# Kernel optimization log

Measured on AMD Instinct MI355X. Metric: run time of the kernel, lower is better.

## Reference

```python
import jax, jax.numpy as jnp
import numpy as np

B, Q, R, D = 32, 512, 1024, 2048
L = Q + R
GAMMA, LMBDA, KL_COEFF = 0.99, 0.95, 0.1
PENALISE_NO_EOS = True
REWARD_PENALTY = -3.0
MIN_RESPONSE_LEN = 0
MAX_RESPONSE_LEN = 1024


def setup_inputs() -> dict:
    key = jax.random.key(0)
    k = jax.random.split(key, 6)
    hidden = jax.random.normal(k[0], (B, L, D), jnp.float32)
    w_base = jax.random.normal(k[1], (D,), jnp.float32) / np.float32(np.sqrt(D))
    w_adapter = jax.random.normal(k[2], (D,), jnp.float32) / np.float32(np.sqrt(D))
    gen_logprobs = jax.random.normal(k[3], (B, R), jnp.float32)
    ref_logprobs = jax.random.normal(k[4], (B, R), jnp.float32)
    # left-aligned responses: resp_lens real tokens then padding (True = pad).
    resp_lens = jax.random.randint(k[5], (B,), 1, R + 1)
    responses_pad_mask = jnp.arange(R)[None, :] >= resp_lens[:, None]
    return {"hidden": hidden, "w_base": w_base, "w_adapter": w_adapter,
            "gen_logprobs": gen_logprobs, "ref_logprobs": ref_logprobs,
            "responses_pad_mask": responses_pad_mask, "queries_len": Q}


def _gae(values, rewards):
    # backward-in-time GAE recurrence via lax.scan (reverse=True), vectorized over batch
    v_next = jnp.concatenate([values[:, 1:], jnp.zeros_like(values[:, :1])], axis=1)
    def step(carry, xs):
        v_t, r_t, vn_t = xs
        adv = r_t + GAMMA * vn_t - v_t + GAMMA * LMBDA * carry
        return adv, adv
    init = jnp.zeros(values.shape[0], values.dtype)
    _, advs = jax.lax.scan(step, init, (values.T, rewards.T, v_next.T), reverse=True)
    return advs.T  # [B, R]


def _masked_whiten(x, mask):
    # torchtune masked_whiten: masked mean/var (Bessel-corrected) over all masked entries
    m = mask.astype(x.dtype)
    n = jnp.sum(m)
    mean = jnp.sum(x * m) / n
    var = jnp.sum(((x - mean) ** 2) * m) / n
    var = var * (n / (n - 1.0))  # unbiased
    return (x - mean) * jax.lax.rsqrt(var + 1e-8)


def _forward(hidden, w_base, w_adapter, gen_logprobs, ref_logprobs,
             responses_pad_mask, queries_len):
    b = hidden.shape[0]
    # scorer with adapter -> values; scorer with adapter disabled -> scores
    values_full = jnp.einsum('bld,d->bl', hidden, w_base + w_adapter)
    scores_full = jnp.einsum('bld,d->bl', hidden, w_base)
    values = values_full[:, queries_len - 1:-1]  # [B, R]

    # index of last unmasked (non-pad) response token; 0 if fully padded
    response_last_pos = jnp.argmax(jnp.cumsum(~responses_pad_mask, axis=-1), axis=-1)

    scores = jnp.take_along_axis(
        scores_full, (response_last_pos + queries_len)[:, None], axis=1)[:, 0]

    penalty_mask = jnp.zeros((b,), bool)
    if PENALISE_NO_EOS:
        penalty_mask = penalty_mask | ~jnp.any(responses_pad_mask, axis=-1)
    if MIN_RESPONSE_LEN:
        penalty_mask = penalty_mask | (response_last_pos < MIN_RESPONSE_LEN)
    scores = jnp.where(penalty_mask, jnp.asarray(REWARD_PENALTY, scores.dtype), scores)

    value_last_pos = jnp.where(
        (response_last_pos > 0) & (response_last_pos < MAX_RESPONSE_LEN - 1),
        response_last_pos + 1, response_last_pos)
    value_pad_mask = responses_pad_mask.at[jnp.arange(b), value_last_pos].set(False)
    values = jnp.where(value_pad_mask, jnp.asarray(0.0, values.dtype), values)

    # get_rewards_ppo
    kl = gen_logprobs - ref_logprobs
    kl_rewards = -KL_COEFF * kl
    rewards = kl_rewards.at[jnp.arange(b), value_last_pos].add(scores)

    # estimate_advantages
    advantages = _gae(values, rewards)
    returns = advantages + values
    mask = ~responses_pad_mask
    advantages = jnp.where(mask, _masked_whiten(advantages, mask),
                           jnp.asarray(0.0, advantages.dtype))

    return (values, value_pad_mask, value_last_pos, scores, response_last_pos,
            kl, kl_rewards, advantages, returns)


def reference(hidden, w_base, w_adapter, gen_logprobs, ref_logprobs,
              responses_pad_mask, queries_len):
    return _forward(hidden, w_base, w_adapter, gen_logprobs, ref_logprobs,
                    responses_pad_mask, queries_len)
```

## Files before the change

kernel.cpp:

```cpp
#include <hip/hip_runtime.h>

#define B_   32
#define Q_   512
#define R_   1024
#define D_   2048
#define L_   1536
#define NROW (B_ * 1025)

#define O_VALUES 0
#define O_VPM    32768
#define O_VLP    65536
#define O_SC     65568
#define O_RLP    65600
#define O_KL     65632
#define O_KLR    98400
#define O_ADV    131168
#define O_RET    163936

__constant__ float kGamma = 0.99f;
__constant__ float kLmbda = 0.95f;

__global__ __launch_bounds__(256) void k_dots(
    const float* __restrict__ hidden,
    const float* __restrict__ wb,
    const float* __restrict__ wa,
    float* __restrict__ vals_dot,
    float* __restrict__ scores_dot)
{
    const int lane = threadIdx.x & 63;
    const int wid  = blockIdx.x * 4 + (threadIdx.x >> 6);
    const int nw   = gridDim.x * 4;

    const float4* wb4 = (const float4*)wb;
    const float4* wa4 = (const float4*)wa;
    float4 vb[8], vs[8];
#pragma unroll
    for (int k = 0; k < 8; ++k) {
        float4 bv = wb4[lane + 64 * k];
        float4 av = wa4[lane + 64 * k];
        vb[k] = bv;
        vs[k] = make_float4(bv.x + av.x, bv.y + av.y, bv.z + av.z, bv.w + av.w);
    }

    for (int row = wid; row < NROW; row += nw) {
        const int bb = row / 1025;
        const int i  = row - bb * 1025;
        const float4* hp =
            (const float4*)(hidden + ((size_t)bb * L_ + 511 + i) * (size_t)D_);
        float4 h[8];
#pragma unroll
        for (int k = 0; k < 8; ++k) h[k] = hp[lane + 64 * k];
        float db = 0.f, ds = 0.f;
#pragma unroll
        for (int k = 0; k < 8; ++k) {
            db += h[k].x * vb[k].x + h[k].y * vb[k].y + h[k].z * vb[k].z + h[k].w * vb[k].w;
            ds += h[k].x * vs[k].x + h[k].y * vs[k].y + h[k].z * vs[k].z + h[k].w * vs[k].w;
        }
#pragma unroll
        for (int d = 32; d > 0; d >>= 1) {
            db += __shfl_down(db, d, 64);
            ds += __shfl_down(ds, d, 64);
        }
        if (lane == 0) { vals_dot[row] = ds; scores_dot[row] = db; }
    }
}

__global__ __launch_bounds__(64) void k_seq(
    const float* __restrict__ vals_dot,
    const float* __restrict__ scores_dot,
    const float* __restrict__ gen,
    const float* __restrict__ ref,
    const void* __restrict__ maskraw,
    float* __restrict__ out,
    double* __restrict__ acc,
    int* __restrict__ flag)
{
    const int b    = blockIdx.x;
    const int lane = threadIdx.x;

    bool oddNZ = false;
    const unsigned int* mu = (const unsigned int*)maskraw;
    for (int j = lane; j < (B_ * R_) / 4; j += 64) {
        if (mu[j] & 0xFFFFFF00u) oddNZ = true;
    }
    const bool byteMode = (__ballot(oddNZ) != 0ull);
    if (b == 0 && lane == 0) *flag = byteMode ? 1 : 0;

    const int base = b * R_ + lane * 16;
    bool m[16];
    if (byteMode) {
        const unsigned char* mb = (const unsigned char*)maskraw;
#pragma unroll
        for (int j = 0; j < 16; ++j) m[j] = mb[base + j] != 0;
    } else {
        const int* mi = (const int*)maskraw;
#pragma unroll
        for (int j = 0; j < 16; ++j) m[j] = mi[base + j] != 0;
    }

    int  ll   = -1;
    bool anyT = false;
#pragma unroll
    for (int j = 0; j < 16; ++j) {
        if (!m[j]) ll = lane * 16 + j;
        anyT |= m[j];
    }
#pragma unroll
    for (int d = 1; d < 64; d <<= 1) {
        int o = __shfl_xor(ll, d, 64);
        ll = ll > o ? ll : o;
    }
    int rlp = ll < 0 ? 0 : ll;
    const bool anyPad = (__ballot(anyT) != 0ull);
    const float score = (!anyPad) ? -3.0f : scores_dot[b * 1025 + rlp + 1];
    const int vlp = (rlp > 0 && rlp < R_ - 1) ? rlp + 1 : rlp;

    float v[16];
#pragma unroll
    for (int j = 0; j < 16; ++j) {
        const int t = lane * 16 + j;
        const bool vpm = m[j] && (t != vlp);
        const float vv = vpm ? 0.f : vals_dot[b * 1025 + t];
        v[j] = vv;
        out[O_VALUES + b * R_ + t] = vv;
        out[O_VPM + b * R_ + t]    = vpm ? 1.f : 0.f;
    }
    float tshf = __shfl_down(v[0], 1, 64);
    const float vnext_head = (lane == 63) ? 0.f : tshf;

    const float c = kGamma * kLmbda;
    float dl[16];
#pragma unroll
    for (int j = 0; j < 16; ++j) {
        const int t = lane * 16 + j;
        const float kl = gen[b * R_ + t] - ref[b * R_ + t];
        out[O_KL + b * R_ + t]  = kl;
        const float klr = -0.1f * kl;
        out[O_KLR + b * R_ + t] = klr;
        const float rw = klr + ((t == vlp) ? score : 0.f);
        const float vn = (j < 15) ? v[j + 1] : vnext_head;
        dl[j] = rw + kGamma * vn - v[j];
    }

    float a[16];
    a[15] = dl[15];
#pragma unroll
    for (int j = 14; j >= 0; --j) a[j] = dl[j] + c * a[j + 1];

    const float c2 = c * c, c4 = c2 * c2, c8 = c4 * c4, c16 = c8 * c8;
    float S = a[0];
    float f = c16;
#pragma unroll
    for (int d = 1; d < 64; d <<= 1) {
        float up = __shfl_down(S, d, 64);
        up = (lane + d < 64) ? up : 0.f;
        S += f * up;
        f *= f;
    }
    float t1 = __shfl_down(S, 1, 64);
    float carry = (lane == 63) ? 0.f : t1;
#pragma unroll
    for (int j = 15; j >= 0; --j) {
        a[j] = dl[j] + c * carry;
        carry = a[j];
    }

    double sx = 0.0, sx2 = 0.0, n = 0.0;
#pragma unroll
    for (int j = 0; j < 16; ++j) {
        const int t = lane * 16 + j;
        out[O_ADV + b * R_ + t] = a[j];
        out[O_RET + b * R_ + t] = a[j] + v[j];
        if (!m[j]) { sx += (double)a[j]; sx2 += (double)a[j] * (double)a[j]; n += 1.0; }
    }
#pragma unroll
    for (int d = 1; d < 64; d <<= 1) {
        sx  += __shfl_xor(sx, d, 64);
        sx2 += __shfl_xor(sx2, d, 64);
        n   += __shfl_xor(n, d, 64);
    }
    if (lane == 0) {
        atomicAdd(&acc[0], sx);
        atomicAdd(&acc[1], sx2);
        atomicAdd(&acc[2], n);
        out[O_VLP + b] = (float)vlp;
        out[O_SC + b]  = score;
        out[O_RLP + b] = (float)rlp;
    }
}

__global__ __launch_bounds__(256) void k_whiten(
    float* __restrict__ out,
    const double* __restrict__ acc,
    const void* __restrict__ maskraw,
    const int* __restrict__ flag)
{
    const int i = blockIdx.x * blockDim.x + threadIdx.x;
    if (i >= B_ * R_) return;
    const double sx = acc[0], sx2 = acc[1], n = acc[2];
    const double mean = sx / n;
    const double var  = (sx2 - sx * sx / n) / (n - 1.0);
    const float  rs   = (float)(1.0 / sqrt(var + 1e-8));
    bool pad;
    if (*flag) pad = ((const unsigned char*)maskraw)[i] != 0;
    else       pad = ((const int*)maskraw)[i] != 0;
    const float x = out[O_ADV + i];
    out[O_ADV + i] = pad ? 0.f : (x - (float)mean) * rs;
}

extern "C" void kernel_launch(void* const* d_in, const int* in_sizes, int n_in,
                              void* d_out, int out_size, void* d_ws, size_t ws_size,
                              hipStream_t stream) {
    const float* hidden = (const float*)d_in[0];
    const float* wb     = (const float*)d_in[1];
    const float* wa     = (const float*)d_in[2];
    const float* gen    = (const float*)d_in[3];
    const float* ref    = (const float*)d_in[4];
    const void*  mask   = d_in[5];

    float* out = (float*)d_out;
    float* wsf = (float*)d_ws;
    float* vals_dot   = wsf;
    float* scores_dot = wsf + NROW;
    double* acc = (double*)((char*)d_ws + (size_t)2 * NROW * sizeof(float));
    int* flag   = (int*)((char*)d_ws + (size_t)2 * NROW * sizeof(float) + 3 * sizeof(double));

    hipMemsetAsync((char*)d_ws + (size_t)2 * NROW * sizeof(float), 0,
                   3 * sizeof(double) + sizeof(int), stream);

    hipLaunchKernelGGL(k_dots, dim3(2048), dim3(256), 0, stream,
                       hidden, wb, wa, vals_dot, scores_dot);
    hipLaunchKernelGGL(k_seq, dim3(B_), dim3(64), 0, stream,
                       vals_dot, scores_dot, gen, ref, mask, out, acc, flag);
    hipLaunchKernelGGL(k_whiten, dim3((B_ * R_ + 255) / 256), dim3(256), 0, stream,
                       out, acc, mask, flag);
}
```

Before: 533.7 us.

## Skip dot products past each response end and fuse GAE with whitening

A new single-block prep kernel computes each row's last response position, value position, pad flag and the mask format up front. The dot-product kernel uses this to skip hidden rows beyond rlp+1. Those rows are either masked to zero or never read, so most of the dominant hidden-state read for padded tokens goes away. The per-batch GAE kernel and the separate whitening kernel are merged into one 1024-thread block that reduces statistics in shared memory, which removes the double atomics and the memset. The cost is that the scan and whitening now run on a single workgroup, and there is an extra launch plus a dependency on the metadata.

```diff
diff --git a/kernel.cpp b/kernel.cpp
--- a/kernel.cpp
+++ b/kernel.cpp
@@ -17,13 +17,75 @@
 #define O_ADV    131168
 #define O_RET    163936
 
-__constant__ float kGamma = 0.99f;
-__constant__ float kLmbda = 0.95f;
+#define M_FLAG 0
+#define M_RLP  1
+#define M_VLP  33
+#define M_PAD  65
+#define M_LIM  97
+
+__global__ __launch_bounds__(1024) void k_prep(
+    const void* __restrict__ maskraw,
+    int* __restrict__ meta)
+{
+    __shared__ int sflag;
+    const int tid = threadIdx.x;
+    if (tid == 0) sflag = 0;
+    __syncthreads();
+
+    const unsigned int* mu = (const unsigned int*)maskraw;
+    bool odd = false;
+    for (int j = tid; j < (B_ * R_) / 4; j += 1024)
+        odd |= (mu[j] & 0xFFFFFF00u) != 0u;
+    if (odd) atomicOr(&sflag, 1);
+    __syncthreads();
+    const int byteMode = sflag;
+
+    const int w = tid >> 6, lane = tid & 63;
+    for (int p = 0; p < 2; ++p) {
+        const int b = w + 16 * p;
+        const int base = b * R_ + lane * 16;
+        int  ll   = -1;
+        bool anyT = false;
+        if (byteMode) {
+            const unsigned char* mb = (const unsigned char*)maskraw;
+#pragma unroll
+            for (int j = 0; j < 16; ++j) {
+                const bool m = mb[base + j] != 0;
+                if (!m) ll = lane * 16 + j;
+                anyT |= m;
+            }
+        } else {
+            const int* mi = (const int*)maskraw;
+#pragma unroll
+            for (int j = 0; j < 16; ++j) {
+                const bool m = mi[base + j] != 0;
+                if (!m) ll = lane * 16 + j;
+                anyT |= m;
+            }
+        }
+#pragma unroll
+        for (int d = 1; d < 64; d <<= 1) {
+            int o = __shfl_xor(ll, d, 64);
+            ll = ll > o ? ll : o;
+        }
+        const int  rlp    = ll < 0 ? 0 : ll;
+        const bool anyPad = (__ballot(anyT) != 0ull);
+        const int  vlp    = (rlp > 0 && rlp < R_ - 1) ? rlp + 1 : rlp;
+        if (lane == 0) {
+            meta[M_RLP + b] = rlp;
+            meta[M_VLP + b] = vlp;
+            meta[M_PAD + b] = anyPad ? 1 : 0;
+            meta[M_LIM + b] = rlp + 1;
+        }
+    }
+    if (tid == 0) meta[M_FLAG] = byteMode;
+}
 
 __global__ __launch_bounds__(256) void k_dots(
     const float* __restrict__ hidden,
     const float* __restrict__ wb,
     const float* __restrict__ wa,
+    const int*   __restrict__ meta,
     float* __restrict__ vals_dot,
     float* __restrict__ scores_dot)
 {
@@ -45,6 +107,7 @@
     for (int row = wid; row < NROW; row += nw) {
         const int bb = row / 1025;
         const int i  = row - bb * 1025;
+        if (i > meta[M_LIM + bb]) continue;
         const float4* hp =
             (const float4*)(hidden + ((size_t)bb * L_ + 511 + i) * (size_t)D_);
         float4 h[8];
@@ -65,147 +128,140 @@
     }
 }
 
-__global__ __launch_bounds__(64) void k_seq(
+__global__ __launch_bounds__(1024) void k_seq2(
     const float* __restrict__ vals_dot,
     const float* __restrict__ scores_dot,
     const float* __restrict__ gen,
     const float* __restrict__ ref,
-    const void* __restrict__ maskraw,
-    float* __restrict__ out,
-    double* __restrict__ acc,
-    int* __restrict__ flag)
+    const void*  __restrict__ maskraw,
+    const int*   __restrict__ meta,
+    float* __restrict__ out)
 {
-    const int b    = blockIdx.x;
-    const int lane = threadIdx.x;
-
-    bool oddNZ = false;
-    const unsigned int* mu = (const unsigned int*)maskraw;
-    for (int j = lane; j < (B_ * R_) / 4; j += 64) {
-        if (mu[j] & 0xFFFFFF00u) oddNZ = true;
-    }
-    const bool byteMode = (__ballot(oddNZ) != 0ull);
-    if (b == 0 && lane == 0) *flag = byteMode ? 1 : 0;
-
-    const int base = b * R_ + lane * 16;
-    bool m[16];
-    if (byteMode) {
-        const unsigned char* mb = (const unsigned char*)maskraw;
-#pragma unroll
-        for (int j = 0; j < 16; ++j) m[j] = mb[base + j] != 0;
-    } else {
-        const int* mi = (const int*)maskraw;
-#pragma unroll
-        for (int j = 0; j < 16; ++j) m[j] = mi[base + j] != 0;
-    }
-
-    int  ll   = -1;
-    bool anyT = false;
-#pragma unroll
-    for (int j = 0; j < 16; ++j) {
-        if (!m[j]) ll = lane * 16 + j;
-        anyT |= m[j];
-    }
-#pragma unroll
-    for (int d = 1; d < 64; d <<= 1) {
-        int o = __shfl_xor(ll, d, 64);
-        ll = ll > o ? ll : o;
-    }
-    int rlp = ll < 0 ? 0 : ll;
-    const bool anyPad = (__ballot(anyT) != 0ull);
-    const float score = (!anyPad) ? -3.0f : scores_dot[b * 1025 + rlp + 1];
-    const int vlp = (rlp > 0 && rlp < R_ - 1) ? rlp + 1 : rlp;
-
-    float v[16];
-#pragma unroll
-    for (int j = 0; j < 16; ++j) {
-        const int t = lane * 16 + j;
-        const bool vpm = m[j] && (t != vlp);
-        const float vv = vpm ? 0.f : vals_dot[b * 1025 + t];
-        v[j] = vv;
-        out[O_VALUES + b * R_ + t] = vv;
-        out[O_VPM + b * R_ + t]    = vpm ? 1.f : 0.f;
-    }
-    float tshf = __shfl_down(v[0], 1, 64);
-    const float vnext_head = (lane == 63) ? 0.f : tshf;
-
-    const float c = kGamma * kLmbda;
-    float dl[16];
-#pragma unroll
-    for (int j = 0; j < 16; ++j) {
-        const int t = lane * 16 + j;
-        const float kl = gen[b * R_ + t] - ref[b * R_ + t];
-        out[O_KL + b * R_ + t]  = kl;
-        const float klr = -0.1f * kl;
-        out[O_KLR + b * R_ + t] = klr;
-        const float rw = klr + ((t == vlp) ? score : 0.f);
-        const float vn = (j < 15) ? v[j + 1] : vnext_head;
-        dl[j] = rw + kGamma * vn - v[j];
-    }
-
-    float a[16];
-    a[15] = dl[15];
-#pragma unroll
-    for (int j = 14; j >= 0; --j) a[j] = dl[j] + c * a[j + 1];
-
+    __shared__ double red0[16], red1[16], red2[16];
+    __shared__ float  smean, srs;
+
+    const int tid  = threadIdx.x;
+    const int w    = tid >> 6, lane = tid & 63;
+    const int byteMode = meta[M_FLAG];
+
+    const float c  = 0.99f * 0.95f;
     const float c2 = c * c, c4 = c2 * c2, c8 = c4 * c4, c16 = c8 * c8;
-    float S = a[0];
-    float f = c16;
-#pragma unroll
-    for (int d = 1; d < 64; d <<= 1) {
-        float up = __shfl_down(S, d, 64);
-        up = (lane + d < 64) ? up : 0.f;
-        S += f * up;
-        f *= f;
-    }
-    float t1 = __shfl_down(S, 1, 64);
-    float carry = (lane == 63) ? 0.f : t1;
-#pragma unroll
-    for (int j = 15; j >= 0; --j) {
-        a[j] = dl[j] + c * carry;
-        carry = a[j];
-    }
-
-    double sx = 0.0, sx2 = 0.0, n = 0.0;
-#pragma unroll
-    for (int j = 0; j < 16; ++j) {
-        const int t = lane * 16 + j;
-        out[O_ADV + b * R_ + t] = a[j];
-        out[O_RET + b * R_ + t] = a[j] + v[j];
-        if (!m[j]) { sx += (double)a[j]; sx2 += (double)a[j] * (double)a[j]; n += 1.0; }
-    }
+
+    float        aP[2][16];
+    unsigned int pm[2];
+    double sx = 0.0, sx2 = 0.0, nn = 0.0;
+
+    for (int p = 0; p < 2; ++p) {
+        const int b      = w + 16 * p;
+        const int rlp    = meta[M_RLP + b];
+        const int vlp    = meta[M_VLP + b];
+        const int anyPad = meta[M_PAD + b];
+        const int base   = b * R_ + lane * 16;
+
+        unsigned int mbits = 0;
+        if (byteMode) {
+            const unsigned char* mb = (const unsigned char*)maskraw;
+#pragma unroll
+            for (int j = 0; j < 16; ++j) mbits |= (mb[base + j] ? 1u : 0u) << j;
+        } else {
+            const int* mi = (const int*)maskraw;
+#pragma unroll
+            for (int j = 0; j < 16; ++j) mbits |= (mi[base + j] ? 1u : 0u) << j;
+        }
+        pm[p] = mbits;
+
+        const float score = anyPad ? scores_dot[b * 1025 + rlp + 1] : -3.0f;
+
+        float v[16], dl[16];
+#pragma unroll
+        for (int j = 0; j < 16; ++j) {
+            const int  t   = lane * 16 + j;
+            const bool mj  = (mbits >> j) & 1u;
+            const bool vpm = mj && (t != vlp);
+            const float vv = vpm ? 0.f : vals_dot[b * 1025 + t];
+            v[j] = vv;
+            out[O_VALUES + b * R_ + t] = vv;
+            out[O_VPM + b * R_ + t]    = vpm ? 1.f : 0.f;
+        }
+        float tsh = __shfl_down(v[0], 1, 64);
+        const float vnh = (lane == 63) ? 0.f : tsh;
+
+#pragma unroll
+        for (int j = 0; j < 16; ++j) {
+            const int t = lane * 16 + j;
+            const float kl = gen[b * R_ + t] - ref[b * R_ + t];
+            out[O_KL + b * R_ + t] = kl;
+            const float klr = -0.1f * kl;
+            out[O_KLR + b * R_ + t] = klr;
+            const float rw = klr + ((t == vlp) ? score : 0.f);
+            const float vn = (j < 15) ? v[j + 1] : vnh;
+            dl[j] = rw + 0.99f * vn - v[j];
+        }
+
+        float a[16];
+        a[15] = dl[15];
+#pragma unroll
+        for (int j = 14; j >= 0; --j) a[j] = dl[j] + c * a[j + 1];
+
+        float S = a[0], f = c16;
+#pragma unroll
+        for (int d = 1; d < 64; d <<= 1) {
+            float up = __shfl_down(S, d, 64);
+            up = (lane + d < 64) ? up : 0.f;
+            S += f * up;
+            f *= f;
+        }
+        float t1 = __shfl_down(S, 1, 64);
+        float carry = (lane == 63) ? 0.f : t1;
+#pragma unroll
+        for (int j = 15; j >= 0; --j) { a[j] = dl[j] + c * carry; carry = a[j]; }
+
+#pragma unroll
+        for (int j = 0; j < 16; ++j) {
+            const int t = lane * 16 + j;
+            out[O_RET + b * R_ + t] = a[j] + v[j];
+            aP[p][j] = a[j];
+            if (!((mbits >> j) & 1u)) {
+                sx  += (double)a[j];
+                sx2 += (double)a[j] * (double)a[j];
+                nn  += 1.0;
+            }
+        }
+        if (lane == 0) {
+            out[O_VLP + b] = (float)vlp;
+            out[O_SC + b]  = score;
+            out[O_RLP + b] = (float)rlp;
+        }
+    }
+
 #pragma unroll
     for (int d = 1; d < 64; d <<= 1) {
         sx  += __shfl_xor(sx, d, 64);
         sx2 += __shfl_xor(sx2, d, 64);
-        n   += __shfl_xor(n, d, 64);
-    }
-    if (lane == 0) {
-        atomicAdd(&acc[0], sx);
-        atomicAdd(&acc[1], sx2);
-        atomicAdd(&acc[2], n);
-        out[O_VLP + b] = (float)vlp;
-        out[O_SC + b]  = score;
-        out[O_RLP + b] = (float)rlp;
-    }
-}
-
-__global__ __launch_bounds__(256) void k_whiten(
-    float* __restrict__ out,
-    const double* __restrict__ acc,
-    const void* __restrict__ maskraw,
-    const int* __restrict__ flag)
-{
-    const int i = blockIdx.x * blockDim.x + threadIdx.x;
-    if (i >= B_ * R_) return;
-    const double sx = acc[0], sx2 = acc[1], n = acc[2];
-    const double mean = sx / n;
-    const double var  = (sx2 - sx * sx / n) / (n - 1.0);
-    const float  rs   = (float)(1.0 / sqrt(var + 1e-8));
-    bool pad;
-    if (*flag) pad = ((const unsigned char*)maskraw)[i] != 0;
-    else       pad = ((const int*)maskraw)[i] != 0;
-    const float x = out[O_ADV + i];
-    out[O_ADV + i] = pad ? 0.f : (x - (float)mean) * rs;
+        nn  += __shfl_xor(nn, d, 64);
+    }
+    if (lane == 0) { red0[w] = sx; red1[w] = sx2; red2[w] = nn; }
+    __syncthreads();
+    if (tid == 0) {
+        double SX = 0.0, SX2 = 0.0, N = 0.0;
+        for (int i = 0; i < 16; ++i) { SX += red0[i]; SX2 += red1[i]; N += red2[i]; }
+        const double mean = SX / N;
+        const double var  = (SX2 - SX * SX / N) / (N - 1.0);
+        smean = (float)mean;
+        srs   = (float)(1.0 / sqrt(var + 1e-8));
+    }
+    __syncthreads();
+    const float mean = smean, rsc = srs;
+
+    for (int p = 0; p < 2; ++p) {
+        const int b = w + 16 * p;
+#pragma unroll
+        for (int j = 0; j < 16; ++j) {
+            const int t = lane * 16 + j;
+            const bool mj = (pm[p] >> j) & 1u;
+            out[O_ADV + b * R_ + t] = mj ? 0.f : (aP[p][j] - mean) * rsc;
+        }
+    }
 }
 
 extern "C" void kernel_launch(void* const* d_in, const int* in_sizes, int n_in,
@@ -222,16 +278,11 @@
     float* wsf = (float*)d_ws;
     float* vals_dot   = wsf;
     float* scores_dot = wsf + NROW;
-    double* acc = (double*)((char*)d_ws + (size_t)2 * NROW * sizeof(float));
-    int* flag   = (int*)((char*)d_ws + (size_t)2 * NROW * sizeof(float) + 3 * sizeof(double));
-
-    hipMemsetAsync((char*)d_ws + (size_t)2 * NROW * sizeof(float), 0,
-                   3 * sizeof(double) + sizeof(int), stream);
-
+    int*   meta       = (int*)((char*)d_ws + (size_t)2 * NROW * sizeof(float));
+
+    hipLaunchKernelGGL(k_prep, dim3(1), dim3(1024), 0, stream, mask, meta);
     hipLaunchKernelGGL(k_dots, dim3(2048), dim3(256), 0, stream,
-                       hidden, wb, wa, vals_dot, scores_dot);
-    hipLaunchKernelGGL(k_seq, dim3(B_), dim3(64), 0, stream,
-                       vals_dot, scores_dot, gen, ref, mask, out, acc, flag);
-    hipLaunchKernelGGL(k_whiten, dim3((B_ * R_ + 255) / 256), dim3(256), 0, stream,
-                       out, acc, mask, flag);
-}
+                       hidden, wb, wa, meta, vals_dot, scores_dot);
+    hipLaunchKernelGGL(k_seq2, dim3(1), dim3(1024), 0, stream,
+                       vals_dot, scores_dot, gen, ref, mask, meta, out);
+}
```

Result: slower. 564.0 us (+5.7%).
